# Kernel tuning notes

Measured on AMD Instinct MI355X. Metric: run time of the kernel, lower is better.

Reference implementation:

```python
import jax, jax.numpy as jnp
import numpy as np

N, E, B = 4096, 32768, 64
F_IN, E_FEAT, D, D3, G = 128, 64, 64, 64, 10
L = 3           # gc_count
SIG = 0.15      # prior_sig
LAMDA = 0.01    # DiffGroupNorm lambda
EPS = 1e-5      # BatchNorm eps


def setup_inputs() -> dict:
    key = jax.random.key(0)
    ks = jax.random.split(key, 24)
    u = lambda k, shape, s=0.02: jax.random.uniform(k, shape, jnp.float32, -s, s)
    return {
        "x": jax.random.normal(ks[0], (N, F_IN), jnp.float32),
        "edge_attr": jax.random.normal(ks[1], (E, E_FEAT), jnp.float32),
        "pre_W": u(ks[2], (F_IN, D)),
        "pre_b": u(ks[3], (D,)),
        "edge_w1": u(ks[4], (L, E_FEAT, D3), 0.1),
        "edge_b1": u(ks[5], (L, D3), 0.1),
        "edge_w2": u(ks[6], (L, D3, D * D), 0.05),
        "edge_b2": u(ks[7], (L, D * D), 0.05),
        "root_w": u(ks[8], (L, D, D), 0.1),
        "root_b": u(ks[9], (L, D), 0.1),
        "gru_wih": u(ks[10], (L, 3 * D, D), 0.1),
        "gru_whh": u(ks[11], (L, 3 * D, D), 0.1),
        "gru_bih": u(ks[12], (L, 3 * D), 0.1),
        "gru_bhh": u(ks[13], (L, 3 * D), 0.1),
        "gn_lin": u(ks[14], (L, D, G), 0.1),
        "gn_gamma": jnp.ones((L, G * D), jnp.float32),
        "gn_beta": jnp.zeros((L, G * D), jnp.float32),
        "post_W": u(ks[15], (D, D)),
        "post_b": u(ks[16], (D,)),
        "out_W": u(ks[17], (D, 1)),
        "out_b": u(ks[18], (1,)),
        "edge_index": jax.random.randint(ks[19], (2, E), 0, N),
        "batch": jnp.sort(jax.random.randint(ks[20], (N,), 0, B)),
    }


def _kld_det(W, b):
    # BayesLinear forward with sample=False: closed-form prior term
    logc = jnp.log(SIG * jnp.sqrt(2.0 * np.pi))
    return (0.5 * (W / SIG) ** 2 + logc).sum() + (0.5 * (b / SIG) ** 2 + logc).sum()


def _seg_mean(v, idx, num):
    s = jax.ops.segment_sum(v, idx, num_segments=num)
    c = jax.ops.segment_sum(jnp.ones((v.shape[0],), v.dtype), idx, num_segments=num)
    return s / jnp.clip(c, 1.0)[:, None]


def _gru_cell(m, h, wih, whh, bih, bhh):
    # torch GRU gate order: r, z, n
    gi = m @ wih.T + bih          # [N, 3D]
    gh = h @ whh.T + bhh
    i_r, i_z, i_n = jnp.split(gi, 3, axis=-1)
    h_r, h_z, h_n = jnp.split(gh, 3, axis=-1)
    r = jax.nn.sigmoid(i_r + h_r)
    z = jax.nn.sigmoid(i_z + h_z)
    n = jnp.tanh(i_n + r * h_n)
    return (1.0 - z) * n + z * h


def _diff_group_norm(m, lin, gamma, beta):
    # PyG DiffGroupNorm: x + lamda * sum_g s[:,g] * BN(s*x)
    s = jax.nn.softmax(m @ lin, axis=-1)           # [N, G]
    t = (s[:, :, None] * m[:, None, :]).reshape(m.shape[0], G * D)  # [N, G*D]
    mu = t.mean(axis=0)
    var = t.var(axis=0)                            # biased, as BatchNorm1d training
    tn = (t - mu) / jnp.sqrt(var + EPS) * gamma + beta
    return m + LAMDA * tn.reshape(m.shape[0], G, D).sum(axis=1)


def reference(x, edge_attr, pre_W, pre_b, edge_w1, edge_b1, edge_w2, edge_b2,
              root_w, root_b, gru_wih, gru_whh, gru_bih, gru_bhh,
              gn_lin, gn_gamma, gn_beta, post_W, post_b, out_W, out_b,
              edge_index, batch):
    src, dst = edge_index[0], edge_index[1]

    # pre FC (BayesLinear, sample=False) + relu
    out = jax.nn.relu(x @ pre_W + pre_b)
    tkl = _kld_det(pre_W, pre_b)
    prev = out
    h = out                                         # GRU hidden state

    for i in range(L):
        # edge-conditioned weights: MLP(edge_attr) -> [E, D, D]
        We = (jax.nn.relu(edge_attr @ edge_w1[i] + edge_b1[i]) @ edge_w2[i]
              + edge_b2[i]).reshape(E, D, D)
        msg = jnp.einsum('ef,efo->eo', out[src], We)        # gather + per-edge matmul
        agg = _seg_mean(msg, dst, N)                        # scatter-mean
        m = agg + out @ root_w[i] + root_b[i]               # NNConv root weight + bias
        m = _diff_group_norm(m, gn_lin[i], gn_gamma[i], gn_beta[i])
        m = jax.nn.relu(m)
        h = _gru_cell(m, h, gru_wih[i], gru_whh[i], gru_bih[i], gru_bhh[i])
        out = h + prev                                      # residual
        prev = out

    # early global_mean_pool over graphs
    pooled = _seg_mean(out, batch, B)                       # [B, D]
    p = jax.nn.relu(pooled @ post_W + post_b)
    tkl = tkl + _kld_det(post_W, post_b)
    y = p @ out_W + out_b                                   # [B, 1]
    tkl = tkl + _kld_det(out_W, out_b)
    return y.reshape(-1), tkl
```

## Files before the change

kernel.cpp:

```cpp
#include <hip/hip_runtime.h>
#include <math.h>

#define Nn 4096
#define Ee 32768
#define Bb 64
#define FINc 128
#define Dd 64
#define SIGf 0.15f
#define LAMf 0.01f
#define EPSf 1e-5f

typedef __attribute__((ext_vector_type(8))) short bf16x8;
typedef __attribute__((ext_vector_type(4))) float f32x4;

__device__ inline short f2bf(float f) {
  union { float f; unsigned u; } v; v.f = f;
  unsigned r = v.u + 0x7fffu + ((v.u >> 16) & 1u);
  return (short)(r >> 16);
}
__device__ inline float bf2f(unsigned short s) {
  union { unsigned u; float f; } v; v.u = ((unsigned)s) << 16; return v.f;
}
__device__ inline bf16x8 pack8v(f32x4 a, f32x4 b) {
  bf16x8 r;
  r[0]=f2bf(a.x); r[1]=f2bf(a.y); r[2]=f2bf(a.z); r[3]=f2bf(a.w);
  r[4]=f2bf(b.x); r[5]=f2bf(b.y); r[6]=f2bf(b.z); r[7]=f2bf(b.w);
  return r;
}
__device__ inline float sigm(float x) { return 1.f / (1.f + expf(-x)); }

__global__ __launch_bounds__(256) void k_prep(
    const float* __restrict__ w1, const float* __restrict__ w2,
    const float* __restrict__ b2, const float* __restrict__ rootw,
    const float* __restrict__ gwih, const float* __restrict__ gwhh,
    const float* __restrict__ preW, const float* __restrict__ preb,
    const float* __restrict__ postW, const float* __restrict__ postb,
    const float* __restrict__ outW, const float* __restrict__ outb,
    const int* __restrict__ dstIdx,
    short* __restrict__ w1T, short* __restrict__ b2T,
    short* __restrict__ w2T, short* __restrict__ rootwT,
    short* __restrict__ gwihB, short* __restrict__ gwhhB,
    short* __restrict__ preWT, float* __restrict__ cnt,
    float* __restrict__ y) {
  const int tid = threadIdx.x;
  const int bid = blockIdx.x;
  __shared__ float tile[64][65];
  __shared__ float red[256];

  if (bid < 192) {
    const float* srcp = w2 + (size_t)bid*4096;
    #pragma unroll
    for (int r = 0; r < 16; ++r) {
      int i2 = r*256 + tid;
      tile[i2 >> 6][i2 & 63] = srcp[i2];
    }
    __syncthreads();
    short* dstp = w2T + (size_t)bid*4096;
    #pragma unroll
    for (int r = 0; r < 16; ++r) {
      int i2 = r*256 + tid;
      dstp[i2] = f2bf(tile[i2 & 63][i2 >> 6]);
    }
  } else if (bid < 336) {
    int idx = (bid - 192)*256 + tid;
    if (idx < 3*64*64) {
      int f = idx & 63, h = (idx >> 6) & 63, l = idx >> 12;
      w1T[idx] = f2bf(w1[l*4096 + f*64 + h]);
      b2T[idx] = f2bf(b2[l*4096 + f*64 + h]);
      rootwT[idx] = f2bf(rootw[l*4096 + f*64 + h]);
    }
    if (idx < 3*192*64) {
      gwihB[idx] = f2bf(gwih[idx]);
      gwhhB[idx] = f2bf(gwhh[idx]);
    }
    if (idx < 64*128) {
      int k = idx & 127, d = idx >> 7;
      preWT[idx] = f2bf(preW[k*64 + d]);
    }
    if (idx < Ee) atomicAdd(&cnt[dstIdx[idx]], 1.0f);
  } else {
    const float logc = logf(SIGf * sqrtf(6.28318530717958647692f));
    const float c2 = 0.5f / (SIGf * SIGf);
    float acc = 0.f;
    for (int i = tid; i < FINc*Dd; i += 256) { float w = preW[i];  acc += c2*w*w + logc; }
    for (int i = tid; i < Dd; i += 256)      { float w = preb[i];  acc += c2*w*w + logc; }
    for (int i = tid; i < Dd*Dd; i += 256)   { float w = postW[i]; acc += c2*w*w + logc; }
    for (int i = tid; i < Dd; i += 256)      { float w = postb[i]; acc += c2*w*w + logc; }
    for (int i = tid; i < Dd; i += 256)      { float w = outW[i];  acc += c2*w*w + logc; }
    if (tid == 0)                            { float w = outb[0];  acc += c2*w*w + logc; }
    red[tid] = acc; __syncthreads();
    for (int s = 128; s > 0; s >>= 1) { if (tid < s) red[tid] += red[tid+s]; __syncthreads(); }
    if (tid == 0) y[Bb] = red[0];
  }
}

__global__ __launch_bounds__(256) void k_pre(const float* __restrict__ x,
                                             const short* __restrict__ preWT,
                                             const float* __restrict__ preb,
                                             float* __restrict__ out, float* __restrict__ h) {
  const int tid = threadIdx.x, lane = tid & 63, wave = tid >> 6;
  const int m15 = lane & 15, kq = lane >> 4;
  const int nb = blockIdx.x * 16;
  const f32x4 zero4 = {0.f,0.f,0.f,0.f};
  const int d = wave*16 + m15;
  bf16x8 bfr[4];
  #pragma unroll
  for (int c = 0; c < 4; ++c)
    bfr[c] = *(const bf16x8*)(preWT + d*128 + c*32 + kq*8);
  const float* xp = x + (size_t)(nb + m15)*128 + kq*8;
  f32x4 p = zero4;
  #pragma unroll
  for (int c = 0; c < 4; ++c) {
    bf16x8 a = pack8v(*(const f32x4*)(xp + c*32), *(const f32x4*)(xp + c*32 + 4));
    p = __builtin_amdgcn_mfma_f32_16x16x32_bf16(a, bfr[c], p, 0, 0, 0);
  }
  float bv = preb[d];
  #pragma unroll
  for (int r = 0; r < 4; ++r) {
    int node = nb + kq*4 + r;
    float v = fmaxf(p[r] + bv, 0.f);
    out[node*64 + d] = v;
    h[node*64 + d] = v;
  }
}

__global__ __launch_bounds__(128) void k_msg(
    const float* __restrict__ out, const float* __restrict__ edge_attr,
    const short* __restrict__ w1T, const float* __restrict__ b1,
    const short* __restrict__ w2T, const short* __restrict__ b2T,
    const int* __restrict__ src, const int* __restrict__ dst,
    float* __restrict__ agg, float* __restrict__ stats) {
  __shared__ short hidT[64*136];
  __shared__ __align__(16) short wstage[8192];
  __shared__ int srcv[128];
  __shared__ int dstv[128];

  const int tid  = threadIdx.x;
  const int lane = tid & 63;
  const int w    = tid >> 6;
  const int m15  = lane & 15;
  const int kq   = lane >> 4;
  const int ebi  = blockIdx.x & 255;
  const int os   = blockIdx.x >> 8;
  const int ebase = ebi * 128;
  const int we   = w*64;

  srcv[tid] = src[ebase + tid];
  dstv[tid] = dst[ebase + tid];
  if (blockIdx.x == 0) {
    for (int i = tid; i < 1280; i += 128) stats[i] = 0.f;
  }
  __syncthreads();

  const f32x4 zero4 = {0.f, 0.f, 0.f, 0.f};

  f32x4 s0, s1, s2, s3, s4, s5, s6, s7;
  {
    const short* pg = w2T + (size_t)(w*4)*4096 + os*1024 + lane*16;
    s0 = *(const f32x4*)(pg);          s1 = *(const f32x4*)(pg + 8);
    s2 = *(const f32x4*)(pg + 4096);   s3 = *(const f32x4*)(pg + 4104);
    s4 = *(const f32x4*)(pg + 8192);   s5 = *(const f32x4*)(pg + 8200);
    s6 = *(const f32x4*)(pg + 12288);  s7 = *(const f32x4*)(pg + 12296);
  }
  const int wb0 = (lane*32) ^ ((((lane*32) >> 7) & 7) << 4);
  const int wb1 = (lane*32 + 16) ^ ((((lane*32) >> 7) & 7) << 4);

  bf16x8 sfrag[4][2];
  #pragma unroll
  for (int t = 0; t < 4; ++t) {
    int node = srcv[we + t*16 + m15];
    const float* sp = out + node*64 + kq*8;
    #pragma unroll
    for (int ks = 0; ks < 2; ++ks)
      sfrag[t][ks] = pack8v(*(const f32x4*)(sp + ks*32), *(const f32x4*)(sp + ks*32 + 4));
  }

  {
    bf16x8 ea[4][2];
    #pragma unroll
    for (int t = 0; t < 4; ++t) {
      const float* ep = edge_attr + (size_t)(ebase + we + t*16 + m15)*64 + kq*8;
      ea[t][0] = pack8v(*(const f32x4*)(ep),      *(const f32x4*)(ep + 4));
      ea[t][1] = pack8v(*(const f32x4*)(ep + 32), *(const f32x4*)(ep + 36));
    }
    #pragma unroll
    for (int hg = 0; hg < 4; ++hg) {
      const short* wp = w1T + (hg*16 + m15)*64 + kq*8;
      bf16x8 bw0 = *(const bf16x8*)(wp);
      bf16x8 bw1 = *(const bf16x8*)(wp + 32);
      float b1v = b1[hg*16 + m15];
      #pragma unroll
      for (int t = 0; t < 4; ++t) {
        f32x4 p = __builtin_amdgcn_mfma_f32_16x16x32_bf16(ea[t][0], bw0, zero4, 0, 0, 0);
        p = __builtin_amdgcn_mfma_f32_16x16x32_bf16(ea[t][1], bw1, p, 0, 0, 0);
        ushort4 hp4;
        hp4.x = (unsigned short)f2bf(fmaxf(p.x + b1v, 0.f));
        hp4.y = (unsigned short)f2bf(fmaxf(p.y + b1v, 0.f));
        hp4.z = (unsigned short)f2bf(fmaxf(p.z + b1v, 0.f));
        hp4.w = (unsigned short)f2bf(fmaxf(p.w + b1v, 0.f));
        *(ushort4*)(hidT + (hg*16 + m15)*136 + we + t*16 + kq*4) = hp4;
      }
    }
  }

  f32x4 acc[4] = {zero4, zero4, zero4, zero4};
  const int ro0 = (m15*128 + kq*16) ^ ((m15 & 7) << 4);
  const int ro1 = (m15*128 + 64 + kq*16) ^ ((m15 & 7) << 4);

  for (int c = 0; c < 8; ++c) {
    __syncthreads();
    {
      char* wd = (char*)wstage + (w*4)*2048;
      *(f32x4*)(wd + wb0) = s0;          *(f32x4*)(wd + wb1) = s1;
      *(f32x4*)(wd + 2048 + wb0) = s2;   *(f32x4*)(wd + 2048 + wb1) = s3;
      *(f32x4*)(wd + 4096 + wb0) = s4;   *(f32x4*)(wd + 4096 + wb1) = s5;
      *(f32x4*)(wd + 6144 + wb0) = s6;   *(f32x4*)(wd + 6144 + wb1) = s7;
    }
    __syncthreads();
    if (c < 7) {
      const short* pg = w2T + (size_t)((c + 1)*8 + w*4)*4096 + os*1024 + lane*16;
      s0 = *(const f32x4*)(pg);          s1 = *(const f32x4*)(pg + 8);
      s2 = *(const f32x4*)(pg + 4096);   s3 = *(const f32x4*)(pg + 4104);
      s4 = *(const f32x4*)(pg + 8192);   s5 = *(const f32x4*)(pg + 8200);
      s6 = *(const f32x4*)(pg + 12288);  s7 = *(const f32x4*)(pg + 12296);
    }
    #pragma unroll 2
    for (int j = 0; j < 8; ++j) {
      const char* wbp = (const char*)wstage + j*2048;
      bf16x8 W0 = *(const bf16x8*)(wbp + ro0);
      bf16x8 W1 = *(const bf16x8*)(wbp + ro1);
      const unsigned short* hrow =
          (const unsigned short*)hidT + (c*8 + j)*136 + we + kq*4;
      #pragma unroll
      for (int t = 0; t < 4; ++t) {
        f32x4 p = __builtin_amdgcn_mfma_f32_16x16x32_bf16(sfrag[t][0], W0, zero4, 0, 0, 0);
        p = __builtin_amdgcn_mfma_f32_16x16x32_bf16(sfrag[t][1], W1, p, 0, 0, 0);
        ushort4 hu = *(const ushort4*)(hrow + t*16);
        acc[t].x += bf2f(hu.x) * p.x;
        acc[t].y += bf2f(hu.y) * p.y;
        acc[t].z += bf2f(hu.z) * p.z;
        acc[t].w += bf2f(hu.w) * p.w;
      }
    }
  }

  {
    const short* Bp = b2T + (os*16 + m15)*64 + kq*8;
    bf16x8 W0 = *(const bf16x8*)(Bp);
    bf16x8 W1 = *(const bf16x8*)(Bp + 32);
    #pragma unroll
    for (int t = 0; t < 4; ++t) {
      f32x4 p = __builtin_amdgcn_mfma_f32_16x16x32_bf16(sfrag[t][0], W0, zero4, 0, 0, 0);
      p = __builtin_amdgcn_mfma_f32_16x16x32_bf16(sfrag[t][1], W1, p, 0, 0, 0);
      acc[t] += p;
    }
  }

  #pragma unroll
  for (int t = 0; t < 4; ++t) {
    #pragma unroll
    for (int r = 0; r < 4; ++r) {
      int e = we + t*16 + kq*4 + r;
      atomicAdd(&agg[((size_t)os*Nn + dstv[e])*16 + m15], acc[t][r]);
    }
  }
}

__global__ __launch_bounds__(256) void k_m_fused(
    float* __restrict__ agg, const float* __restrict__ cnt,
    const float* __restrict__ out, const short* __restrict__ rootwT,
    const float* __restrict__ rootb, const float* __restrict__ gnlin,
    float* __restrict__ m, float* __restrict__ sbuf, float* __restrict__ stats) {
  __shared__ float msh[16*65];
  __shared__ float lgsh[16*12];
  __shared__ float ssh[16*16];
  const int tid = threadIdx.x, lane = tid & 63, wave = tid >> 6;
  const int m15 = lane & 15, kq = lane >> 4;
  const int nb = blockIdx.x * 16;
  const f32x4 zero4 = {0.f,0.f,0.f,0.f};
  const int d = wave*16 + m15;

  bf16x8 b0 = *(const bf16x8*)(rootwT + d*64 + kq*8);
  bf16x8 b1 = *(const bf16x8*)(rootwT + d*64 + 32 + kq*8);
  float rbv = rootb[d];
  {
    const float* sp = out + (size_t)(nb + m15)*64 + kq*8;
    bf16x8 a0 = pack8v(*(const f32x4*)(sp),      *(const f32x4*)(sp + 4));
    bf16x8 a1 = pack8v(*(const f32x4*)(sp + 32), *(const f32x4*)(sp + 36));
    f32x4 p = __builtin_amdgcn_mfma_f32_16x16x32_bf16(a0, b0, zero4, 0, 0, 0);
    p = __builtin_amdgcn_mfma_f32_16x16x32_bf16(a1, b1, p, 0, 0, 0);
    #pragma unroll
    for (int r = 0; r < 4; ++r) {
      int ln = kq*4 + r;
      int node = nb + ln;
      size_t ai = ((size_t)wave*Nn + node)*16 + m15;
      float av = agg[ai];
      agg[ai] = 0.f;
      float mv = av / fmaxf(cnt[node], 1.f) + rbv + p[r];
      m[node*64 + d] = mv;
      msh[ln*65 + d] = mv;
    }
  }
  __syncthreads();

  {
    int n = tid >> 4, g = tid & 15;
    if (g < 10) {
      float lg = 0.f;
      #pragma unroll 8
      for (int k = 0; k < 64; ++k) lg += msh[n*65 + k] * gnlin[k*10 + g];
      lgsh[n*12 + g] = lg;
    }
  }
  __syncthreads();
  {
    int n = tid >> 4, g = tid & 15;
    if (g < 10) {
      float mx = -1e30f;
      #pragma unroll
      for (int gg = 0; gg < 10; ++gg) mx = fmaxf(mx, lgsh[n*12 + gg]);
      float sum = 0.f;
      #pragma unroll
      for (int gg = 0; gg < 10; ++gg) sum += expf(lgsh[n*12 + gg] - mx);
      float sv = expf(lgsh[n*12 + g] - mx) / sum;
      sbuf[(nb + n)*16 + g] = sv;
      ssh[n*16 + g] = sv;
    }
  }
  __syncthreads();
  for (int c = tid; c < 640; c += 256) {
    int g = c >> 6, dd = c & 63;
    float a1 = 0.f, a2 = 0.f;
    #pragma unroll
    for (int n = 0; n < 16; ++n) {
      float t = ssh[n*16 + g] * msh[n*65 + dd];
      a1 += t; a2 += t*t;
    }
    atomicAdd(&stats[c], a1);
    atomicAdd(&stats[640 + c], a2);
  }
}

__global__ __launch_bounds__(256) void k_gru(
    const float* __restrict__ m, const float* __restrict__ sbuf,
    const float* __restrict__ stats, const float* __restrict__ gamma,
    const float* __restrict__ beta, const short* __restrict__ gwihB,
    const short* __restrict__ gwhhB, const float* __restrict__ bih,
    const float* __restrict__ bhh, float* __restrict__ h,
    float* __restrict__ out,
    const int* __restrict__ batch, float* __restrict__ pooled,
    float* __restrict__ pcnt, int doPool) {
  __shared__ __align__(16) float mrsh[16*68];
  __shared__ float igsh[640];
  __shared__ float Bsh[64];
  __shared__ float ssh[256];
  const int tid = threadIdx.x, lane = tid & 63, wave = tid >> 6;
  const int m15 = lane & 15, kq = lane >> 4;
  const int nb = blockIdx.x * 16;
  const f32x4 zero4 = {0.f,0.f,0.f,0.f};
  const float invN = 1.f / (float)Nn;

  if (tid < 64) {
    float bacc = 0.f;
    #pragma unroll
    for (int g = 0; g < 10; ++g) {
      int c = g*64 + tid;
      float mu = stats[c] * invN;
      float var = stats[640 + c] * invN - mu*mu;
      float ig = (1.0f / sqrtf(var + EPSf)) * gamma[c];
      igsh[c] = ig;
      bacc += beta[c] - mu * ig;
    }
    Bsh[tid] = bacc;
  }
  ssh[tid] = sbuf[nb*16 + tid];
  __syncthreads();

  for (int idx = tid; idx < 1024; idx += 256) {
    int n = idx >> 6, dd = idx & 63;
    float mv = m[(nb + n)*64 + dd];
    float SA = 0.f;
    #pragma unroll
    for (int g = 0; g < 10; ++g) SA += ssh[n*16 + g] * igsh[g*64 + dd];
    mrsh[n*68 + dd] = fmaxf(mv * (1.f + LAMf*SA) + LAMf*Bsh[dd], 0.f);
  }
  __syncthreads();

  bf16x8 mrf[2], hf[2];
  {
    const float* mp = mrsh + m15*68 + kq*8;
    const float* hp = h + (size_t)(nb + m15)*64 + kq*8;
    #pragma unroll
    for (int ks = 0; ks < 2; ++ks) {
      mrf[ks] = pack8v(*(const f32x4*)(mp + ks*32), *(const f32x4*)(mp + ks*32 + 4));
      hf[ks]  = pack8v(*(const f32x4*)(hp + ks*32), *(const f32x4*)(hp + ks*32 + 4));
    }
  }
  const int d = wave*16 + m15;
  f32x4 gi[3], gh[3];
  #pragma unroll
  for (int p = 0; p < 3; ++p) {
    int j = p*64 + d;
    bf16x8 bi0 = *(const bf16x8*)(gwihB + j*64 + kq*8);
    bf16x8 bi1 = *(const bf16x8*)(gwihB + j*64 + 32 + kq*8);
    bf16x8 bh0 = *(const bf16x8*)(gwhhB + j*64 + kq*8);
    bf16x8 bh1 = *(const bf16x8*)(gwhhB + j*64 + 32 + kq*8);
    f32x4 a = __builtin_amdgcn_mfma_f32_16x16x32_bf16(mrf[0], bi0, zero4, 0, 0, 0);
    gi[p] = __builtin_amdgcn_mfma_f32_16x16x32_bf16(mrf[1], bi1, a, 0, 0, 0);
    f32x4 b = __builtin_amdgcn_mfma_f32_16x16x32_bf16(hf[0], bh0, zero4, 0, 0, 0);
    gh[p] = __builtin_amdgcn_mfma_f32_16x16x32_bf16(hf[1], bh1, b, 0, 0, 0);
  }
  float bir = bih[d],      bhr = bhh[d];
  float biz = bih[64 + d], bhz = bhh[64 + d];
  float bin = bih[128 + d], bhn = bhh[128 + d];
  __syncthreads();
  #pragma unroll
  for (int r = 0; r < 4; ++r) {
    int node = nb + kq*4 + r;
    float rr = sigm(gi[0][r] + bir + gh[0][r] + bhr);
    float z  = sigm(gi[1][r] + biz + gh[1][r] + bhz);
    float nn = tanhf(gi[2][r] + bin + rr * (gh[2][r] + bhn));
    float hv = h[node*64 + d];
    float hn = (1.f - z) * nn + z * hv;
    h[node*64 + d] = hn;
    float ov = hn + out[node*64 + d];
    out[node*64 + d] = ov;
    if (doPool) {
      int b = batch[node];
      atomicAdd(&pooled[b*64 + d], ov);
      if (d == 0) atomicAdd(&pcnt[b], 1.f);
    }
  }
}

__global__ void k_final(const float* __restrict__ pooled, const float* __restrict__ pcnt,
                        const float* __restrict__ postW, const float* __restrict__ postb,
                        const float* __restrict__ outW, const float* __restrict__ outb,
                        float* __restrict__ y) {
  int b = blockIdx.x, d = threadIdx.x;
  __shared__ float pl[64];
  float c = fmaxf(pcnt[b], 1.f);
  pl[d] = pooled[b*64 + d] / c;
  __syncthreads();
  float acc = postb[d];
  #pragma unroll 8
  for (int k = 0; k < 64; ++k) acc += pl[k] * postW[k*64 + d];
  acc = fmaxf(acc, 0.f);
  float v = acc * outW[d];
  #pragma unroll
  for (int off = 32; off > 0; off >>= 1) v += __shfl_down(v, off, 64);
  if (d == 0) y[b] = v + outb[0];
}

extern "C" void kernel_launch(void* const* d_in, const int* in_sizes, int n_in,
                              void* d_out, int out_size, void* d_ws, size_t ws_size,
                              hipStream_t stream) {
  (void)in_sizes; (void)n_in; (void)out_size; (void)ws_size;
  const float* x        = (const float*)d_in[0];
  const float* edge_attr= (const float*)d_in[1];
  const float* preW     = (const float*)d_in[2];
  const float* preb     = (const float*)d_in[3];
  const float* ew1      = (const float*)d_in[4];
  const float* eb1      = (const float*)d_in[5];
  const float* ew2      = (const float*)d_in[6];
  const float* eb2      = (const float*)d_in[7];
  const float* rootw    = (const float*)d_in[8];
  const float* rootb    = (const float*)d_in[9];
  const float* gwih     = (const float*)d_in[10];
  const float* gwhh     = (const float*)d_in[11];
  const float* gbih     = (const float*)d_in[12];
  const float* gbhh     = (const float*)d_in[13];
  const float* gnlin    = (const float*)d_in[14];
  const float* gngamma  = (const float*)d_in[15];
  const float* gnbeta   = (const float*)d_in[16];
  const float* postW    = (const float*)d_in[17];
  const float* postb    = (const float*)d_in[18];
  const float* outW     = (const float*)d_in[19];
  const float* outb     = (const float*)d_in[20];
  const int*   eidx     = (const int*)d_in[21];
  const int*   batch    = (const int*)d_in[22];
  const int* src = eidx;
  const int* dst = eidx + Ee;
  float* y = (float*)d_out;

  float* ws     = (float*)d_ws;
  float* out    = ws;
  float* hbuf   = out    + Nn*64;
  float* mbuf   = hbuf   + Nn*64;
  float* sbuf   = mbuf   + Nn*64;
  float* agg    = sbuf   + Nn*16;
  float* stats  = agg    + Nn*64;
  float* cnt    = stats  + 2048;
  float* pooled = cnt    + Nn;
  float* pcnt   = pooled + Nn;
  float* bfbase = pcnt   + 64;
  short* w1T    = (short*)bfbase;
  short* b2T    = w1T    + 3*4096;
  short* w2T    = b2T    + 3*4096;
  short* rootwT = w2T    + 3*262144;
  short* gwihB  = rootwT + 3*4096;
  short* gwhhB  = gwihB  + 3*12288;
  short* preWT  = gwhhB  + 3*12288;

  hipMemsetAsync(agg, 0, (Nn*64 + 2048 + Nn + Nn + 64)*sizeof(float), stream);

  k_prep<<<337, 256, 0, stream>>>(ew1, ew2, eb2, rootw, gwih, gwhh, preW, preb,
                                  postW, postb, outW, outb, dst,
                                  w1T, b2T, w2T, rootwT, gwihB, gwhhB, preWT,
                                  cnt, y);
  k_pre<<<Nn/16, 256, 0, stream>>>(x, preWT, preb, out, hbuf);

  for (int i = 0; i < 3; ++i) {
    k_msg<<<(Ee/128)*4, 128, 0, stream>>>(out, edge_attr,
                                     w1T + i*4096, eb1 + i*64,
                                     w2T + i*262144, b2T + i*4096,
                                     src, dst, agg, stats);
    k_m_fused<<<Nn/16, 256, 0, stream>>>(agg, cnt, out, rootwT + i*4096,
                                         rootb + i*64, gnlin + i*640, mbuf, sbuf, stats);
    k_gru<<<Nn/16, 256, 0, stream>>>(mbuf, sbuf, stats, gngamma + i*640, gnbeta + i*640,
                                     gwihB + i*12288, gwhhB + i*12288,
                                     gbih + i*192, gbhh + i*192, hbuf, out,
                                     batch, pooled, pcnt, (i == 2) ? 1 : 0);
  }

  k_final<<<Bb, 64, 0, stream>>>(pooled, pcnt, postW, postb, outW, outb, y);
}
```

Before: 309.0 us.

## Fuse message-norm and GRU kernels using a grid-wide spin barrier

Merges k_m_fused and k_gru into a single k_mgru kernel per layer. Where the old kernel boundary enforced global completion of the group-norm statistics, it now uses an atomic per-layer counter with a spin wait. The m and softmax assignment values stay in shared memory instead of being written to global buffers and reloaded. This removes one launch per layer and a global round trip, but it relies on all 256 blocks being co-resident. The bounded spin guard could also silently continue with incomplete statistics.

New measurement: 382.9 us. 1.24x slower.

```diff
diff --git a/kernel.cpp b/kernel.cpp
--- a/kernel.cpp
+++ b/kernel.cpp
@@ -266,24 +266,33 @@
   }
 }
 
-__global__ __launch_bounds__(256) void k_m_fused(
+__global__ __launch_bounds__(256) void k_mgru(
     float* __restrict__ agg, const float* __restrict__ cnt,
-    const float* __restrict__ out, const short* __restrict__ rootwT,
-    const float* __restrict__ rootb, const float* __restrict__ gnlin,
-    float* __restrict__ m, float* __restrict__ sbuf, float* __restrict__ stats) {
+    const short* __restrict__ rootwT, const float* __restrict__ rootb,
+    const float* __restrict__ gnlin, float* __restrict__ stats,
+    const float* __restrict__ gamma, const float* __restrict__ beta,
+    const short* __restrict__ gwihB, const short* __restrict__ gwhhB,
+    const float* __restrict__ bih, const float* __restrict__ bhh,
+    float* __restrict__ h, float* __restrict__ out,
+    const int* __restrict__ batch, float* __restrict__ pooled,
+    float* __restrict__ pcnt, int doPool, int layer) {
   __shared__ float msh[16*65];
   __shared__ float lgsh[16*12];
   __shared__ float ssh[16*16];
+  __shared__ float igsh[640];
+  __shared__ float Bsh[64];
+  __shared__ __align__(16) float mrsh[16*68];
   const int tid = threadIdx.x, lane = tid & 63, wave = tid >> 6;
   const int m15 = lane & 15, kq = lane >> 4;
   const int nb = blockIdx.x * 16;
   const f32x4 zero4 = {0.f,0.f,0.f,0.f};
+  const float invN = 1.f / (float)Nn;
   const int d = wave*16 + m15;
 
-  bf16x8 b0 = *(const bf16x8*)(rootwT + d*64 + kq*8);
-  bf16x8 b1 = *(const bf16x8*)(rootwT + d*64 + 32 + kq*8);
-  float rbv = rootb[d];
-  {
+  {
+    bf16x8 b0 = *(const bf16x8*)(rootwT + d*64 + kq*8);
+    bf16x8 b1 = *(const bf16x8*)(rootwT + d*64 + 32 + kq*8);
+    float rbv = rootb[d];
     const float* sp = out + (size_t)(nb + m15)*64 + kq*8;
     bf16x8 a0 = pack8v(*(const f32x4*)(sp),      *(const f32x4*)(sp + 4));
     bf16x8 a1 = pack8v(*(const f32x4*)(sp + 32), *(const f32x4*)(sp + 36));
@@ -296,9 +305,7 @@
       size_t ai = ((size_t)wave*Nn + node)*16 + m15;
       float av = agg[ai];
       agg[ai] = 0.f;
-      float mv = av / fmaxf(cnt[node], 1.f) + rbv + p[r];
-      m[node*64 + d] = mv;
-      msh[ln*65 + d] = mv;
+      msh[ln*65 + d] = av / fmaxf(cnt[node], 1.f) + rbv + p[r];
     }
   }
   __syncthreads();
@@ -322,12 +329,11 @@
       float sum = 0.f;
       #pragma unroll
       for (int gg = 0; gg < 10; ++gg) sum += expf(lgsh[n*12 + gg] - mx);
-      float sv = expf(lgsh[n*12 + g] - mx) / sum;
-      sbuf[(nb + n)*16 + g] = sv;
-      ssh[n*16 + g] = sv;
-    }
-  }
-  __syncthreads();
+      ssh[n*16 + g] = expf(lgsh[n*12 + g] - mx) / sum;
+    }
+  }
+  __syncthreads();
+
   for (int c = tid; c < 640; c += 256) {
     int g = c >> 6, dd = c & 63;
     float a1 = 0.f, a2 = 0.f;
@@ -339,46 +345,42 @@
     atomicAdd(&stats[c], a1);
     atomicAdd(&stats[640 + c], a2);
   }
-}
-
-__global__ __launch_bounds__(256) void k_gru(
-    const float* __restrict__ m, const float* __restrict__ sbuf,
-    const float* __restrict__ stats, const float* __restrict__ gamma,
-    const float* __restrict__ beta, const short* __restrict__ gwihB,
-    const short* __restrict__ gwhhB, const float* __restrict__ bih,
-    const float* __restrict__ bhh, float* __restrict__ h,
-    float* __restrict__ out,
-    const int* __restrict__ batch, float* __restrict__ pooled,
-    float* __restrict__ pcnt, int doPool) {
-  __shared__ __align__(16) float mrsh[16*68];
-  __shared__ float igsh[640];
-  __shared__ float Bsh[64];
-  __shared__ float ssh[256];
-  const int tid = threadIdx.x, lane = tid & 63, wave = tid >> 6;
-  const int m15 = lane & 15, kq = lane >> 4;
-  const int nb = blockIdx.x * 16;
-  const f32x4 zero4 = {0.f,0.f,0.f,0.f};
-  const float invN = 1.f / (float)Nn;
+
+  __threadfence();
+  __syncthreads();
+  if (tid == 0) {
+    unsigned int* ctr = (unsigned int*)(stats + 1280) + layer;
+    atomicAdd(ctr, 1u);
+    int guard = 0;
+    while (__hip_atomic_load(ctr, __ATOMIC_RELAXED, __HIP_MEMORY_SCOPE_AGENT) < 256u
+           && guard < 1000000) {
+      ++guard;
+      __builtin_amdgcn_s_sleep(8);
+    }
+    __threadfence();
+  }
+  __syncthreads();
 
   if (tid < 64) {
     float bacc = 0.f;
     #pragma unroll
     for (int g = 0; g < 10; ++g) {
       int c = g*64 + tid;
-      float mu = stats[c] * invN;
-      float var = stats[640 + c] * invN - mu*mu;
+      float s1 = __hip_atomic_load(&stats[c],       __ATOMIC_RELAXED, __HIP_MEMORY_SCOPE_AGENT);
+      float s2 = __hip_atomic_load(&stats[640 + c], __ATOMIC_RELAXED, __HIP_MEMORY_SCOPE_AGENT);
+      float mu = s1 * invN;
+      float var = s2 * invN - mu*mu;
       float ig = (1.0f / sqrtf(var + EPSf)) * gamma[c];
       igsh[c] = ig;
       bacc += beta[c] - mu * ig;
     }
     Bsh[tid] = bacc;
   }
-  ssh[tid] = sbuf[nb*16 + tid];
   __syncthreads();
 
   for (int idx = tid; idx < 1024; idx += 256) {
     int n = idx >> 6, dd = idx & 63;
-    float mv = m[(nb + n)*64 + dd];
+    float mv = msh[n*65 + dd];
     float SA = 0.f;
     #pragma unroll
     for (int g = 0; g < 10; ++g) SA += ssh[n*16 + g] * igsh[g*64 + dd];
@@ -396,7 +398,6 @@
       hf[ks]  = pack8v(*(const f32x4*)(hp + ks*32), *(const f32x4*)(hp + ks*32 + 4));
     }
   }
-  const int d = wave*16 + m15;
   f32x4 gi[3], gh[3];
   #pragma unroll
   for (int p = 0; p < 3; ++p) {
@@ -515,12 +516,12 @@
                                      w1T + i*4096, eb1 + i*64,
                                      w2T + i*262144, b2T + i*4096,
                                      src, dst, agg, stats);
-    k_m_fused<<<Nn/16, 256, 0, stream>>>(agg, cnt, out, rootwT + i*4096,
-                                         rootb + i*64, gnlin + i*640, mbuf, sbuf, stats);
-    k_gru<<<Nn/16, 256, 0, stream>>>(mbuf, sbuf, stats, gngamma + i*640, gnbeta + i*640,
-                                     gwihB + i*12288, gwhhB + i*12288,
-                                     gbih + i*192, gbhh + i*192, hbuf, out,
-                                     batch, pooled, pcnt, (i == 2) ? 1 : 0);
+    k_mgru<<<Nn/16, 256, 0, stream>>>(agg, cnt, rootwT + i*4096, rootb + i*64,
+                                      gnlin + i*640, stats,
+                                      gngamma + i*640, gnbeta + i*640,
+                                      gwihB + i*12288, gwhhB + i*12288,
+                                      gbih + i*192, gbhh + i*192, hbuf, out,
+                                      batch, pooled, pcnt, (i == 2) ? 1 : 0, i);
   }
 
   k_final<<<Bb, 64, 0, stream>>>(pooled, pcnt, postW, postb, outW, outb, y);
```

## Stage edge-MLP weights with direct global-to-LDS loads into a double buffer

Applied to the files above, without the earlier changes.

In the message kernel, the w2 weight chunks no longer travel global → registers → LDS. They are now fetched with `global_load_lds` straight into shared memory. The weight buffer is doubled so the next chunk can land while the current one feeds the MFMA loop, and the XOR swizzle moves from the LDS side to the global address. The goal is to free eight vector registers of staging data, cut one barrier per chunk, and overlap the weight fetch with compute. The cost is twice the weight LDS, and correctness depends on the barrier waiting for the async LDS writes to finish.

After: 336.6 us. 8.9% more time.

```diff
diff --git a/kernel.cpp b/kernel.cpp
--- a/kernel.cpp
+++ b/kernel.cpp
@@ -28,6 +28,12 @@
   return r;
 }
 __device__ inline float sigm(float x) { return 1.f / (1.f + expf(-x)); }
+
+__device__ inline void stage16(const void* g, void* l) {
+  __builtin_amdgcn_global_load_lds(
+      (const __attribute__((address_space(1))) void*)g,
+      (__attribute__((address_space(3))) void*)l, 16, 0, 0);
+}
 
 __global__ __launch_bounds__(256) void k_prep(
     const float* __restrict__ w1, const float* __restrict__ w2,
@@ -131,7 +137,7 @@
     const int* __restrict__ src, const int* __restrict__ dst,
     float* __restrict__ agg, float* __restrict__ stats) {
   __shared__ short hidT[64*136];
-  __shared__ __align__(16) short wstage[8192];
+  __shared__ __align__(16) short wstage[2][8192];
   __shared__ int srcv[128];
   __shared__ int dstv[128];
 
@@ -154,16 +160,17 @@
 
   const f32x4 zero4 = {0.f, 0.f, 0.f, 0.f};
 
-  f32x4 s0, s1, s2, s3, s4, s5, s6, s7;
-  {
-    const short* pg = w2T + (size_t)(w*4)*4096 + os*1024 + lane*16;
-    s0 = *(const f32x4*)(pg);          s1 = *(const f32x4*)(pg + 8);
-    s2 = *(const f32x4*)(pg + 4096);   s3 = *(const f32x4*)(pg + 4104);
-    s4 = *(const f32x4*)(pg + 8192);   s5 = *(const f32x4*)(pg + 8200);
-    s6 = *(const f32x4*)(pg + 12288);  s7 = *(const f32x4*)(pg + 12296);
-  }
-  const int wb0 = (lane*32) ^ ((((lane*32) >> 7) & 7) << 4);
-  const int wb1 = (lane*32 + 16) ^ ((((lane*32) >> 7) & 7) << 4);
+  const int soff = (lane*16) ^ (((lane >> 3) & 7) << 4);
+  const char* gwbase = (const char*)w2T + (size_t)(w*4)*8192 + (size_t)os*2048 + soff;
+
+  {
+    char* lb = (char*)&wstage[0][w*4*1024];
+    #pragma unroll
+    for (int j2 = 0; j2 < 4; ++j2) {
+      stage16(gwbase + (size_t)j2*8192,        lb + j2*2048);
+      stage16(gwbase + (size_t)j2*8192 + 1024, lb + j2*2048 + 1024);
+    }
+  }
 
   bf16x8 sfrag[4][2];
   #pragma unroll
@@ -202,31 +209,25 @@
       }
     }
   }
+  __syncthreads();
 
   f32x4 acc[4] = {zero4, zero4, zero4, zero4};
   const int ro0 = (m15*128 + kq*16) ^ ((m15 & 7) << 4);
   const int ro1 = (m15*128 + 64 + kq*16) ^ ((m15 & 7) << 4);
 
   for (int c = 0; c < 8; ++c) {
-    __syncthreads();
-    {
-      char* wd = (char*)wstage + (w*4)*2048;
-      *(f32x4*)(wd + wb0) = s0;          *(f32x4*)(wd + wb1) = s1;
-      *(f32x4*)(wd + 2048 + wb0) = s2;   *(f32x4*)(wd + 2048 + wb1) = s3;
-      *(f32x4*)(wd + 4096 + wb0) = s4;   *(f32x4*)(wd + 4096 + wb1) = s5;
-      *(f32x4*)(wd + 6144 + wb0) = s6;   *(f32x4*)(wd + 6144 + wb1) = s7;
-    }
-    __syncthreads();
     if (c < 7) {
-      const short* pg = w2T + (size_t)((c + 1)*8 + w*4)*4096 + os*1024 + lane*16;
-      s0 = *(const f32x4*)(pg);          s1 = *(const f32x4*)(pg + 8);
-      s2 = *(const f32x4*)(pg + 4096);   s3 = *(const f32x4*)(pg + 4104);
-      s4 = *(const f32x4*)(pg + 8192);   s5 = *(const f32x4*)(pg + 8200);
-      s6 = *(const f32x4*)(pg + 12288);  s7 = *(const f32x4*)(pg + 12296);
+      const char* gn = gwbase + (size_t)(c + 1)*65536;
+      char* lb = (char*)&wstage[(c + 1) & 1][w*4*1024];
+      #pragma unroll
+      for (int j2 = 0; j2 < 4; ++j2) {
+        stage16(gn + (size_t)j2*8192,        lb + j2*2048);
+        stage16(gn + (size_t)j2*8192 + 1024, lb + j2*2048 + 1024);
+      }
     }
     #pragma unroll 2
     for (int j = 0; j < 8; ++j) {
-      const char* wbp = (const char*)wstage + j*2048;
+      const char* wbp = (const char*)&wstage[c & 1][0] + j*2048;
       bf16x8 W0 = *(const bf16x8*)(wbp + ro0);
       bf16x8 W1 = *(const bf16x8*)(wbp + ro1);
       const unsigned short* hrow =
@@ -242,6 +243,7 @@
         acc[t].w += bf2f(hu.w) * p.w;
       }
     }
+    __syncthreads();
   }
 
   {
```
